# Kernel tuning notes

Measured on AMD Instinct MI355X. Metric: run time of the kernel, lower is better.

Reference implementation:

```python
import jax, jax.numpy as jnp
import numpy as np

B, C, D, K = 65536, 128, 32, 10
EPS = 1e-12


def setup_inputs() -> dict:
    key = jax.random.key(0)
    k1, k2, k3, k4 = jax.random.split(key, 4)
    data = jax.random.normal(k1, (B, D), dtype=jnp.float32)
    mu = jax.random.normal(k2, (C, D), dtype=jnp.float32)
    # S_inv must be symmetric positive definite (inverse covariance per cluster)
    A = 0.1 * jax.random.normal(k3, (C, D, D), dtype=jnp.float32)
    S_inv = jnp.einsum('cij,ckj->cik', A, A) + jnp.eye(D, dtype=jnp.float32)[None]
    # one-hot class assignment per cluster (int32), as stored in the module
    cls = jax.random.randint(k4, (C,), 0, K)
    cluster_labels = jax.nn.one_hot(cls, K, dtype=jnp.int32)
    return {"data": data, "mu": mu, "S_inv": S_inv, "cluster_labels": cluster_labels}


def reference(data, mu, S_inv, cluster_labels):
    # Mahalanobis distance d2[b,c] = (z_b - mu_c)^T S_inv_c (z_b - mu_c),
    # expanded to avoid a [B, C, D] diff tensor.
    zz = data[:, :, None] * data[:, None, :]            # [B, D, D]
    t1 = jnp.einsum('bde,cde->bc', zz, S_inv)           # z' Sinv z
    Sm = jnp.einsum('cde,ce->cd', S_inv, mu)            # [C, D]
    t2 = data @ Sm.T                                    # z' Sinv mu  [B, C]
    t3 = jnp.einsum('cd,cd->c', mu, Sm)                 # mu' Sinv mu [C]
    d2 = t1 - 2.0 * t2 + t3[None, :]                    # [B, C]
    Gamma = jnp.exp(-0.5 * d2)                          # Gaussian activation
    # defuzzify_batch: normalize activations, project through one-hot labels
    norm_gamma = Gamma / (jnp.sum(Gamma, axis=1, keepdims=True) + EPS)
    label_scores = norm_gamma @ cluster_labels.astype(jnp.float32)  # [B, K]
    preds = jnp.argmax(label_scores, axis=1)
    clusters = jnp.argmax(Gamma, axis=1)
    return label_scores, preds, clusters
```

## Files before the change

### kernel.cpp

```cpp
#include <hip/hip_runtime.h>
#include <cmath>

#define B_N 65536
#define C_N 128
#define D_N 32
#define K_N 10
#define EPS_F 1e-12f
#define SCALE_F (-0.72134752044448169f)

#define NKK 46
#define CHUNK_F16 4096
#define QF_N (NKK * CHUNK_F16)
#define YSTR 41

typedef _Float16 f16x8 __attribute__((ext_vector_type(8)));
typedef float    f32x16 __attribute__((ext_vector_type(16)));

__device__ __forceinline__ void mdkk(int kk, int& dA, int& e0) {
    if (kk >= 45) { dA = 0; e0 = 0; return; }
    int w = (kk >= 17) + (kk >= 30) + (kk >= 39) + (kk >= 44);
    int off = w == 0 ? 0 : (w == 1 ? 17 : (w == 2 ? 30 : (w == 3 ? 39 : 44)));
    int r = kk - off;
    dA = 2 * r;
    e0 = 2 * r + 8 * w;
}

__global__ __launch_bounds__(128) void k_prep(const float* __restrict__ S,
                                              const float* __restrict__ mu,
                                              const int* __restrict__ onehot,
                                              _Float16* __restrict__ QF,
                                              int* __restrict__ cls) {
    const int c = blockIdx.x;
    const int tid = threadIdx.x;
    __shared__ float sSm[D_N];
    __shared__ float st3;

    if (tid < D_N) {
        const float* Sr = S + (size_t)c * (D_N * D_N) + (size_t)tid * D_N;
        const float* mr = mu + (size_t)c * D_N;
        float a0 = 0.f, a1 = 0.f;
#pragma unroll
        for (int e = 0; e < D_N; e += 2) {
            a0 = fmaf(Sr[e + 0], mr[e + 0], a0);
            a1 = fmaf(Sr[e + 1], mr[e + 1], a1);
        }
        sSm[tid] = a0 + a1;
    }
    __syncthreads();
    if (tid == 0) {
        const float* mr = mu + (size_t)c * D_N;
        float a = 0.f;
#pragma unroll
        for (int d = 0; d < D_N; ++d) a = fmaf(mr[d], sSm[d], a);
        st3 = a;
        int cl = 0;
#pragma unroll
        for (int k = 0; k < K_N; ++k)
            if (onehot[c * K_N + k] != 0) cl = k;
        cls[c] = cl;
    }
    __syncthreads();

    if (tid < 2 * NKK) {
        const int kk   = tid >> 1;
        const int half = tid & 1;
        int dA, e0;
        mdkk(kk, dA, e0);
        const int d  = dA + half;
        const int ct = c >> 5;
        const size_t base = (size_t)kk * CHUNK_F16 + ct * 1024
                          + (size_t)(half * 32 + (c & 31)) * 8;
        const float* Sc = S + (size_t)c * (D_N * D_N);
        for (int j = 0; j < 8; ++j) {
            const int e = e0 + j;
            float q = 0.f;
            if (kk < 45 && d <= e && e <= 32) {
                float v;
                if (e < 32)      v = Sc[d * D_N + e] * (d == e ? 1.f : 2.f);
                else if (d < 32) v = -2.f * sSm[d];
                else             v = st3;
                q = SCALE_F * v;
            }
            _Float16 h = (_Float16)q;
            QF[base + j]       = h;
            QF[base + 512 + j] = (_Float16)(q - (float)h);
        }
    }
}

__device__ __forceinline__ void gl_lds16(const void* g, void* l) {
    __builtin_amdgcn_global_load_lds(
        (const __attribute__((address_space(1))) unsigned int*)g,
        (__attribute__((address_space(3))) unsigned int*)l, 16, 0, 0);
}

__device__ __forceinline__ void stage_chunk(const _Float16* __restrict__ QF,
                                            _Float16* __restrict__ dst,
                                            int chunk, int wid, int lane) {
#pragma unroll
    for (int i = 0; i < 2; ++i) {
        const int slot = i * 4 + wid;
        gl_lds16(QF + (size_t)chunk * CHUNK_F16 + slot * 512 + lane * 8,
                 dst + slot * 512);
    }
}

__device__ __forceinline__ void ldy(const float* sy, int ybase, int hioff,
                                    int kk, float& yd, float (&yw)[8]) {
    int dA, e0;
    mdkk(kk, dA, e0);
    yd = sy[ybase + dA + hioff];
#pragma unroll
    for (int j = 0; j < 8; ++j) yw[j] = sy[ybase + e0 + j];
}

__device__ __forceinline__ void step_compute(const _Float16* __restrict__ buf,
                                             int lane, float yd, const float (&yw)[8],
                                             f32x16 (&acc)[4]) {
    const f16x8* qb = (const f16x8*)buf;
    f16x8 qh[4], ql[4];
#pragma unroll
    for (int ct = 0; ct < 4; ++ct) {
        qh[ct] = qb[ct * 128 + lane];
        ql[ct] = qb[ct * 128 + 64 + lane];
    }
    f16x8 ph, pl;
#pragma unroll
    for (int j = 0; j < 8; j += 2) {
        float f0 = yd * yw[j], f1 = yd * yw[j + 1];
        auto h2 = __builtin_amdgcn_cvt_pkrtz(f0, f1);
        float r0 = f0 - (float)h2[0];
        float r1 = f1 - (float)h2[1];
        auto l2 = __builtin_amdgcn_cvt_pkrtz(r0, r1);
        ph[j] = h2[0]; ph[j + 1] = h2[1];
        pl[j] = l2[0]; pl[j + 1] = l2[1];
    }
#pragma unroll
    for (int ct = 0; ct < 4; ++ct)
        acc[ct] = __builtin_amdgcn_mfma_f32_32x32x16_f16(qh[ct], ph, acc[ct], 0, 0, 0);
#pragma unroll
    for (int ct = 0; ct < 4; ++ct)
        acc[ct] = __builtin_amdgcn_mfma_f32_32x32x16_f16(ql[ct], ph, acc[ct], 0, 0, 0);
#pragma unroll
    for (int ct = 0; ct < 4; ++ct)
        acc[ct] = __builtin_amdgcn_mfma_f32_32x32x16_f16(qh[ct], pl, acc[ct], 0, 0, 0);
}

__global__ __launch_bounds__(256, 2) void k_mainv6(const float* __restrict__ data,
                                                   const _Float16* __restrict__ QF,
                                                   const int* __restrict__ clsp,
                                                   float* __restrict__ out) {
    const int tid  = threadIdx.x;
    const int lane = tid & 63;
    const int wid  = tid >> 6;
    const int b0w  = blockIdx.x * 128 + wid * 32;
    const int col  = lane & 31;
    const bool hi  = lane >= 32;

    __shared__ float sy[256 * YSTR + 64];
    __shared__ alignas(16) _Float16 qbuf[2][CHUNK_F16];
    __shared__ int lcls[C_N];
    if (tid < C_N) lcls[tid] = clsp[tid];

    const int ybase = tid * YSTR;
    {
        const float4* p0 = (const float4*)(data + (size_t)(b0w + col) * D_N);
#pragma unroll
        for (int i = 0; i < 8; ++i) {
            float4 v = p0[i];
            sy[ybase + 4 * i + 0] = v.x;
            sy[ybase + 4 * i + 1] = v.y;
            sy[ybase + 4 * i + 2] = v.z;
            sy[ybase + 4 * i + 3] = v.w;
        }
        sy[ybase + 32] = 1.f;
#pragma unroll
        for (int i = 33; i < YSTR; ++i) sy[ybase + i] = 0.f;
        if (tid < 64) sy[256 * YSTR + tid] = 0.f;
    }

    f32x16 acc[4];
#pragma unroll
    for (int ct = 0; ct < 4; ++ct)
#pragma unroll
        for (int g = 0; g < 16; ++g) acc[ct][g] = 0.f;

    stage_chunk(QF, &qbuf[0][0], 0, wid, lane);
    stage_chunk(QF, &qbuf[1][0], 1, wid, lane);
    __syncthreads();

    const int hioff = hi ? 1 : 0;
    float ydA, ywA[8], ydB, ywB[8];
    ldy(sy, ybase, hioff, 0, ydA, ywA);

#pragma clang loop unroll(disable)
    for (int t = 0; t < NKK; t += 2) {
        ldy(sy, ybase, hioff, t + 1, ydB, ywB);
        step_compute(&qbuf[0][0], lane, ydA, ywA, acc);
        __syncthreads();
        if (t + 2 < NKK) stage_chunk(QF, &qbuf[0][0], t + 2, wid, lane);
        ldy(sy, ybase, hioff, t + 2, ydA, ywA);
        step_compute(&qbuf[1][0], lane, ydB, ywB, acc);
        __syncthreads();
        if (t + 3 < NKK) stage_chunk(QF, &qbuf[1][0], t + 3, wid, lane);
    }

    const float hoff = hi ? 4.f : 0.f;
    const int* lc = lcls + (hi ? 4 : 0);
    float sum = 0.f, gmax = -1.f, gcf = 0.f;
    float a0 = 0, a1 = 0, a2 = 0, a3 = 0, a4 = 0, a5 = 0, a6 = 0, a7 = 0, a8 = 0, a9 = 0;
#pragma unroll
    for (int ct = 0; ct < 4; ++ct) {
        float psum = 0.f;
#pragma unroll
        for (int g = 0; g < 16; ++g) {
            float v = acc[ct][g];
            float gm;
            asm("v_exp_f32 %0, %1" : "=v"(gm) : "v"(v));
            const int cbase = ct * 32 + (g & 3) + 8 * (g >> 2);
            int cl = lc[cbase];
            psum += gm;
            float cf = (float)cbase + hoff;
            if (gm > gmax) { gmax = gm; gcf = cf; }
            a0 += (cl == 0) ? gm : 0.f;
            a1 += (cl == 1) ? gm : 0.f;
            a2 += (cl == 2) ? gm : 0.f;
            a3 += (cl == 3) ? gm : 0.f;
            a4 += (cl == 4) ? gm : 0.f;
            a5 += (cl == 5) ? gm : 0.f;
            a6 += (cl == 6) ? gm : 0.f;
            a7 += (cl == 7) ? gm : 0.f;
            a8 += (cl == 8) ? gm : 0.f;
            a9 += (cl == 9) ? gm : 0.f;
        }
        sum += psum;
    }

    sum += __shfl_xor(sum, 32, 64);
    {
        float om = __shfl_xor(gmax, 32, 64);
        float oc = __shfl_xor(gcf, 32, 64);
        bool take = (om > gmax) || (om == gmax && oc < gcf);
        if (take) { gmax = om; gcf = oc; }
    }
    a0 += __shfl_xor(a0, 32, 64);
    a1 += __shfl_xor(a1, 32, 64);
    a2 += __shfl_xor(a2, 32, 64);
    a3 += __shfl_xor(a3, 32, 64);
    a4 += __shfl_xor(a4, 32, 64);
    a5 += __shfl_xor(a5, 32, 64);
    a6 += __shfl_xor(a6, 32, 64);
    a7 += __shfl_xor(a7, 32, 64);
    a8 += __shfl_xor(a8, 32, 64);
    a9 += __shfl_xor(a9, 32, 64);

    if (!hi) {
        const int b = b0w + col;
        float inv = 1.0f / (sum + EPS_F);
        float ls[K_N] = {a0 * inv, a1 * inv, a2 * inv, a3 * inv, a4 * inv,
                         a5 * inv, a6 * inv, a7 * inv, a8 * inv, a9 * inv};
        float best = -1.f;
        int bk = 0;
#pragma unroll
        for (int k = 0; k < K_N; ++k)
            if (ls[k] > best) { best = ls[k]; bk = k; }
        float2* o2 = (float2*)(out + (size_t)b * K_N);
#pragma unroll
        for (int k2 = 0; k2 < K_N / 2; ++k2)
            o2[k2] = make_float2(ls[2 * k2], ls[2 * k2 + 1]);
        out[(size_t)B_N * K_N + b] = (float)bk;
        out[(size_t)B_N * K_N + B_N + b] = gcf;
    }
}

extern "C" void kernel_launch(void* const* d_in, const int* in_sizes, int n_in,
                              void* d_out, int out_size, void* d_ws, size_t ws_size,
                              hipStream_t stream) {
    const float* data   = (const float*)d_in[0];
    const float* mu     = (const float*)d_in[1];
    const float* S      = (const float*)d_in[2];
    const int*   onehot = (const int*)d_in[3];
    float* out = (float*)d_out;

    _Float16* QF  = (_Float16*)d_ws;
    int*      cls = (int*)(QF + QF_N);

    hipLaunchKernelGGL(k_prep, dim3(C_N), dim3(128), 0, stream,
                       S, mu, onehot, QF, cls);
    hipLaunchKernelGGL(k_mainv6, dim3(B_N / 128), dim3(256), 0, stream,
                       data, QF, cls, out);
}
```

Baseline: 106.6 us.

## Deepen LDS staging to four buffers with vmcnt-based partial waits

Replaces the double-buffered chunk staging with a four-slot ring that keeps up to three chunks in flight. Each step waits only on its own loads via s_waitcnt vmcnt plus a raw barrier, not a full __syncthreads drain. It also raises wave priority around the MFMA sequence. The aim is to hide global-to-LDS load latency behind matrix work, at the cost of extra LDS (which may reduce occupancy) and fragile hand-counted vmcnt values.

```diff
diff --git a/kernel.cpp b/kernel.cpp
--- a/kernel.cpp
+++ b/kernel.cpp
@@ -105,6 +105,15 @@
     }
 }
 
+template <int VM>
+__device__ __forceinline__ void sync_chunk() {
+    if constexpr (VM == 4)      asm volatile("s_waitcnt vmcnt(4)" ::: "memory");
+    else if constexpr (VM == 2) asm volatile("s_waitcnt vmcnt(2)" ::: "memory");
+    else                        asm volatile("s_waitcnt vmcnt(0)" ::: "memory");
+    __builtin_amdgcn_s_barrier();
+    __builtin_amdgcn_sched_barrier(0);
+}
+
 __device__ __forceinline__ void ldy(const float* sy, int ybase, int hioff,
                                     int kk, float& yd, float (&yw)[8]) {
     int dA, e0;
@@ -135,6 +144,7 @@
         ph[j] = h2[0]; ph[j + 1] = h2[1];
         pl[j] = l2[0]; pl[j + 1] = l2[1];
     }
+    __builtin_amdgcn_s_setprio(1);
 #pragma unroll
     for (int ct = 0; ct < 4; ++ct)
         acc[ct] = __builtin_amdgcn_mfma_f32_32x32x16_f16(qh[ct], ph, acc[ct], 0, 0, 0);
@@ -144,9 +154,10 @@
 #pragma unroll
     for (int ct = 0; ct < 4; ++ct)
         acc[ct] = __builtin_amdgcn_mfma_f32_32x32x16_f16(qh[ct], pl, acc[ct], 0, 0, 0);
-}
-
-__global__ __launch_bounds__(256, 2) void k_mainv6(const float* __restrict__ data,
+    __builtin_amdgcn_s_setprio(0);
+}
+
+__global__ __launch_bounds__(256, 2) void k_mainv7(const float* __restrict__ data,
                                                    const _Float16* __restrict__ QF,
                                                    const int* __restrict__ clsp,
                                                    float* __restrict__ out) {
@@ -158,7 +169,7 @@
     const bool hi  = lane >= 32;
 
     __shared__ float sy[256 * YSTR + 64];
-    __shared__ alignas(16) _Float16 qbuf[2][CHUNK_F16];
+    __shared__ alignas(16) _Float16 qbuf[4][CHUNK_F16];
     __shared__ int lcls[C_N];
     if (tid < C_N) lcls[tid] = clsp[tid];
 
@@ -187,6 +198,7 @@
 
     stage_chunk(QF, &qbuf[0][0], 0, wid, lane);
     stage_chunk(QF, &qbuf[1][0], 1, wid, lane);
+    stage_chunk(QF, &qbuf[2][0], 2, wid, lane);
     __syncthreads();
 
     const int hioff = hi ? 1 : 0;
@@ -194,16 +206,21 @@
     ldy(sy, ybase, hioff, 0, ydA, ywA);
 
 #pragma clang loop unroll(disable)
-    for (int t = 0; t < NKK; t += 2) {
+    for (int t = 0; t < NKK - 2; t += 2) {
         ldy(sy, ybase, hioff, t + 1, ydB, ywB);
-        step_compute(&qbuf[0][0], lane, ydA, ywA, acc);
-        __syncthreads();
-        if (t + 2 < NKK) stage_chunk(QF, &qbuf[0][0], t + 2, wid, lane);
+        sync_chunk<4>();
+        if (t + 3 < NKK) stage_chunk(QF, &qbuf[(t + 3) & 3][0], t + 3, wid, lane);
+        step_compute(&qbuf[t & 3][0], lane, ydA, ywA, acc);
         ldy(sy, ybase, hioff, t + 2, ydA, ywA);
-        step_compute(&qbuf[1][0], lane, ydB, ywB, acc);
-        __syncthreads();
-        if (t + 3 < NKK) stage_chunk(QF, &qbuf[1][0], t + 3, wid, lane);
-    }
+        sync_chunk<4>();
+        if (t + 4 < NKK) stage_chunk(QF, &qbuf[(t + 4) & 3][0], t + 4, wid, lane);
+        step_compute(&qbuf[(t + 1) & 3][0], lane, ydB, ywB, acc);
+    }
+    ldy(sy, ybase, hioff, NKK - 1, ydB, ywB);
+    sync_chunk<2>();
+    step_compute(&qbuf[(NKK - 2) & 3][0], lane, ydA, ywA, acc);
+    sync_chunk<0>();
+    step_compute(&qbuf[(NKK - 1) & 3][0], lane, ydB, ywB, acc);
 
     const float hoff = hi ? 4.f : 0.f;
     const int* lc = lcls + (hi ? 4 : 0);
@@ -287,6 +304,6 @@
 
     hipLaunchKernelGGL(k_prep, dim3(C_N), dim3(128), 0, stream,
                        S, mu, onehot, QF, cls);
-    hipLaunchKernelGGL(k_mainv6, dim3(B_N / 128), dim3(256), 0, stream,
+    hipLaunchKernelGGL(k_mainv7, dim3(B_N / 128), dim3(256), 0, stream,
                        data, QF, cls, out);
 }
```

After: 108.1 us. About the same (+1.4%).

## Split K across wave pairs with two row-groups per wave and LDS reduction

Applied to the files above, without the earlier changes.

Each wave now handles 64 rows (two 32-row MFMA tiles) over half of the K-chunks, so each Q fragment loaded from LDS feeds twice as many MFMAs. The two K-halves are summed through a shared-memory scratch exchange before the epilogue. The loop uses a single barrier per step with an explicit vmcnt wait, and raises wave priority around the MFMA block. In exchange it doubles the accumulator registers, adds a reduction pass, and leaves half the waves idle during the epilogue.

```diff
diff --git a/kernel.cpp b/kernel.cpp
--- a/kernel.cpp
+++ b/kernel.cpp
@@ -9,9 +9,13 @@
 #define SCALE_F (-0.72134752044448169f)
 
 #define NKK 46
+#define HKK 23
 #define CHUNK_F16 4096
 #define QF_N (NKK * CHUNK_F16)
-#define YSTR 41
+#define YSTR 33
+#define SY_FLOATS (128 * YSTR + 64)
+#define SY_BYTES  (SY_FLOATS * 4)
+#define SMEM_BYTES (2 * 8448 * 4)
 
 typedef _Float16 f16x8 __attribute__((ext_vector_type(8)));
 typedef float    f32x16 __attribute__((ext_vector_type(16)));
@@ -105,8 +109,8 @@
     }
 }
 
-__device__ __forceinline__ void ldy(const float* sy, int ybase, int hioff,
-                                    int kk, float& yd, float (&yw)[8]) {
+__device__ __forceinline__ void ldy1(const float* sy, int ybase, int hioff,
+                                     int kk, float& yd, float (&yw)[8]) {
     int dA, e0;
     mdkk(kk, dA, e0);
     yd = sy[ybase + dA + hioff];
@@ -114,17 +118,8 @@
     for (int j = 0; j < 8; ++j) yw[j] = sy[ybase + e0 + j];
 }
 
-__device__ __forceinline__ void step_compute(const _Float16* __restrict__ buf,
-                                             int lane, float yd, const float (&yw)[8],
-                                             f32x16 (&acc)[4]) {
-    const f16x8* qb = (const f16x8*)buf;
-    f16x8 qh[4], ql[4];
-#pragma unroll
-    for (int ct = 0; ct < 4; ++ct) {
-        qh[ct] = qb[ct * 128 + lane];
-        ql[ct] = qb[ct * 128 + 64 + lane];
-    }
-    f16x8 ph, pl;
+__device__ __forceinline__ void mkphi(float yd, const float (&yw)[8],
+                                      f16x8& ph, f16x8& pl) {
 #pragma unroll
     for (int j = 0; j < 8; j += 2) {
         float f0 = yd * yw[j], f1 = yd * yw[j + 1];
@@ -135,141 +130,212 @@
         ph[j] = h2[0]; ph[j + 1] = h2[1];
         pl[j] = l2[0]; pl[j + 1] = l2[1];
     }
-#pragma unroll
-    for (int ct = 0; ct < 4; ++ct)
-        acc[ct] = __builtin_amdgcn_mfma_f32_32x32x16_f16(qh[ct], ph, acc[ct], 0, 0, 0);
-#pragma unroll
-    for (int ct = 0; ct < 4; ++ct)
-        acc[ct] = __builtin_amdgcn_mfma_f32_32x32x16_f16(ql[ct], ph, acc[ct], 0, 0, 0);
-#pragma unroll
-    for (int ct = 0; ct < 4; ++ct)
-        acc[ct] = __builtin_amdgcn_mfma_f32_32x32x16_f16(qh[ct], pl, acc[ct], 0, 0, 0);
-}
-
-__global__ __launch_bounds__(256, 2) void k_mainv6(const float* __restrict__ data,
+}
+
+__device__ __forceinline__ void step2(const _Float16* __restrict__ buf, int lane,
+                                      float yd0, const float (&yw0)[8],
+                                      float yd1, const float (&yw1)[8],
+                                      f32x16 (&acc0)[4], f32x16 (&acc1)[4]) {
+    const f16x8* qbv = (const f16x8*)buf;
+    f16x8 qh[4], ql[4];
+#pragma unroll
+    for (int ct = 0; ct < 4; ++ct) {
+        qh[ct] = qbv[ct * 128 + lane];
+        ql[ct] = qbv[ct * 128 + 64 + lane];
+    }
+    f16x8 ph0, pl0, ph1, pl1;
+    mkphi(yd0, yw0, ph0, pl0);
+    mkphi(yd1, yw1, ph1, pl1);
+    __builtin_amdgcn_s_setprio(1);
+#pragma unroll
+    for (int ct = 0; ct < 4; ++ct)
+        acc0[ct] = __builtin_amdgcn_mfma_f32_32x32x16_f16(qh[ct], ph0, acc0[ct], 0, 0, 0);
+#pragma unroll
+    for (int ct = 0; ct < 4; ++ct)
+        acc1[ct] = __builtin_amdgcn_mfma_f32_32x32x16_f16(qh[ct], ph1, acc1[ct], 0, 0, 0);
+#pragma unroll
+    for (int ct = 0; ct < 4; ++ct)
+        acc0[ct] = __builtin_amdgcn_mfma_f32_32x32x16_f16(ql[ct], ph0, acc0[ct], 0, 0, 0);
+#pragma unroll
+    for (int ct = 0; ct < 4; ++ct)
+        acc1[ct] = __builtin_amdgcn_mfma_f32_32x32x16_f16(ql[ct], ph1, acc1[ct], 0, 0, 0);
+#pragma unroll
+    for (int ct = 0; ct < 4; ++ct)
+        acc0[ct] = __builtin_amdgcn_mfma_f32_32x32x16_f16(qh[ct], pl0, acc0[ct], 0, 0, 0);
+#pragma unroll
+    for (int ct = 0; ct < 4; ++ct)
+        acc1[ct] = __builtin_amdgcn_mfma_f32_32x32x16_f16(qh[ct], pl1, acc1[ct], 0, 0, 0);
+    __builtin_amdgcn_s_setprio(0);
+}
+
+__global__ __launch_bounds__(256, 2) void k_mainv8(const float* __restrict__ data,
                                                    const _Float16* __restrict__ QF,
                                                    const int* __restrict__ clsp,
                                                    float* __restrict__ out) {
     const int tid  = threadIdx.x;
     const int lane = tid & 63;
     const int wid  = tid >> 6;
-    const int b0w  = blockIdx.x * 128 + wid * 32;
+    const int pair = wid >> 1;
+    const int kh   = wid & 1;
     const int col  = lane & 31;
     const bool hi  = lane >= 32;
-
-    __shared__ float sy[256 * YSTR + 64];
-    __shared__ alignas(16) _Float16 qbuf[2][CHUNK_F16];
+    const int rbase = blockIdx.x * 128 + pair * 64;
+
+    __shared__ __attribute__((aligned(16))) char smem[SMEM_BYTES];
     __shared__ int lcls[C_N];
+    float*    sy = (float*)smem;
+    _Float16* qb = (_Float16*)(smem + SY_BYTES);
+
     if (tid < C_N) lcls[tid] = clsp[tid];
-
-    const int ybase = tid * YSTR;
-    {
-        const float4* p0 = (const float4*)(data + (size_t)(b0w + col) * D_N);
+    if (tid < 128) {
+        const float4* p0 = (const float4*)(data + (size_t)(blockIdx.x * 128 + tid) * D_N);
+        const int yb = tid * YSTR;
 #pragma unroll
         for (int i = 0; i < 8; ++i) {
             float4 v = p0[i];
-            sy[ybase + 4 * i + 0] = v.x;
-            sy[ybase + 4 * i + 1] = v.y;
-            sy[ybase + 4 * i + 2] = v.z;
-            sy[ybase + 4 * i + 3] = v.w;
-        }
-        sy[ybase + 32] = 1.f;
-#pragma unroll
-        for (int i = 33; i < YSTR; ++i) sy[ybase + i] = 0.f;
-        if (tid < 64) sy[256 * YSTR + tid] = 0.f;
-    }
-
-    f32x16 acc[4];
-#pragma unroll
-    for (int ct = 0; ct < 4; ++ct)
-#pragma unroll
-        for (int g = 0; g < 16; ++g) acc[ct][g] = 0.f;
-
-    stage_chunk(QF, &qbuf[0][0], 0, wid, lane);
-    stage_chunk(QF, &qbuf[1][0], 1, wid, lane);
+            sy[yb + 4 * i + 0] = v.x;
+            sy[yb + 4 * i + 1] = v.y;
+            sy[yb + 4 * i + 2] = v.z;
+            sy[yb + 4 * i + 3] = v.w;
+        }
+        sy[yb + 32] = 1.f;
+    }
+    if (tid < 64) sy[128 * YSTR + tid] = 0.f;
+
+    f32x16 acc0[4], acc1[4];
+#pragma unroll
+    for (int ct = 0; ct < 4; ++ct)
+#pragma unroll
+        for (int g = 0; g < 16; ++g) { acc0[ct][g] = 0.f; acc1[ct][g] = 0.f; }
+
+    stage_chunk(QF, qb + 0 * CHUNK_F16, 0,   wid, lane);
+    stage_chunk(QF, qb + 2 * CHUNK_F16, HKK, wid, lane);
     __syncthreads();
 
     const int hioff = hi ? 1 : 0;
-    float ydA, ywA[8], ydB, ywB[8];
-    ldy(sy, ybase, hioff, 0, ydA, ywA);
+    const int yb0 = (pair * 64 + col) * YSTR;
+    const int yb1 = yb0 + 32 * YSTR;
 
 #pragma clang loop unroll(disable)
-    for (int t = 0; t < NKK; t += 2) {
-        ldy(sy, ybase, hioff, t + 1, ydB, ywB);
-        step_compute(&qbuf[0][0], lane, ydA, ywA, acc);
-        __syncthreads();
-        if (t + 2 < NKK) stage_chunk(QF, &qbuf[0][0], t + 2, wid, lane);
-        ldy(sy, ybase, hioff, t + 2, ydA, ywA);
-        step_compute(&qbuf[1][0], lane, ydB, ywB, acc);
-        __syncthreads();
-        if (t + 3 < NKK) stage_chunk(QF, &qbuf[1][0], t + 3, wid, lane);
+    for (int t = 0; t < HKK; ++t) {
+        asm volatile("s_waitcnt vmcnt(0)" ::: "memory");
+        __builtin_amdgcn_s_barrier();
+        __builtin_amdgcn_sched_barrier(0);
+        if (t + 1 < HKK) {
+            stage_chunk(QF, qb + (((t + 1) & 1)) * CHUNK_F16, t + 1, wid, lane);
+            stage_chunk(QF, qb + (2 + ((t + 1) & 1)) * CHUNK_F16, HKK + t + 1, wid, lane);
+        }
+        const int kk = kh * HKK + t;
+        float yd0, yw0[8], yd1, yw1[8];
+        ldy1(sy, yb0, hioff, kk, yd0, yw0);
+        ldy1(sy, yb1, hioff, kk, yd1, yw1);
+        step2(qb + (kh * 2 + (t & 1)) * CHUNK_F16, lane, yd0, yw0, yd1, yw1, acc0, acc1);
+    }
+
+    __syncthreads();
+    float* scr = (float*)smem + pair * 8448;
+    if (kh == 1) {
+#pragma unroll
+        for (int bg = 0; bg < 2; ++bg) {
+            const f32x16* ap = bg ? acc1 : acc0;
+#pragma unroll
+            for (int ct = 0; ct < 4; ++ct)
+#pragma unroll
+                for (int gq = 0; gq < 4; ++gq) {
+                    const int g4 = bg * 16 + ct * 4 + gq;
+                    const int fo = lane * 132 + (((g4 + 2 * lane) & 31) << 2);
+                    *(float4*)(scr + fo) = make_float4(ap[ct][4 * gq + 0], ap[ct][4 * gq + 1],
+                                                       ap[ct][4 * gq + 2], ap[ct][4 * gq + 3]);
+                }
+        }
+    }
+    __syncthreads();
+    if (kh != 0) return;
+
+#pragma unroll
+    for (int bg = 0; bg < 2; ++bg) {
+        f32x16* ap = bg ? acc1 : acc0;
+#pragma unroll
+        for (int ct = 0; ct < 4; ++ct)
+#pragma unroll
+            for (int gq = 0; gq < 4; ++gq) {
+                const int g4 = bg * 16 + ct * 4 + gq;
+                const int fo = lane * 132 + (((g4 + 2 * lane) & 31) << 2);
+                float4 v = *(const float4*)(scr + fo);
+                ap[ct][4 * gq + 0] += v.x; ap[ct][4 * gq + 1] += v.y;
+                ap[ct][4 * gq + 2] += v.z; ap[ct][4 * gq + 3] += v.w;
+            }
     }
 
     const float hoff = hi ? 4.f : 0.f;
     const int* lc = lcls + (hi ? 4 : 0);
-    float sum = 0.f, gmax = -1.f, gcf = 0.f;
-    float a0 = 0, a1 = 0, a2 = 0, a3 = 0, a4 = 0, a5 = 0, a6 = 0, a7 = 0, a8 = 0, a9 = 0;
-#pragma unroll
-    for (int ct = 0; ct < 4; ++ct) {
-        float psum = 0.f;
-#pragma unroll
-        for (int g = 0; g < 16; ++g) {
-            float v = acc[ct][g];
-            float gm;
-            asm("v_exp_f32 %0, %1" : "=v"(gm) : "v"(v));
-            const int cbase = ct * 32 + (g & 3) + 8 * (g >> 2);
-            int cl = lc[cbase];
-            psum += gm;
-            float cf = (float)cbase + hoff;
-            if (gm > gmax) { gmax = gm; gcf = cf; }
-            a0 += (cl == 0) ? gm : 0.f;
-            a1 += (cl == 1) ? gm : 0.f;
-            a2 += (cl == 2) ? gm : 0.f;
-            a3 += (cl == 3) ? gm : 0.f;
-            a4 += (cl == 4) ? gm : 0.f;
-            a5 += (cl == 5) ? gm : 0.f;
-            a6 += (cl == 6) ? gm : 0.f;
-            a7 += (cl == 7) ? gm : 0.f;
-            a8 += (cl == 8) ? gm : 0.f;
-            a9 += (cl == 9) ? gm : 0.f;
-        }
-        sum += psum;
-    }
-
-    sum += __shfl_xor(sum, 32, 64);
-    {
-        float om = __shfl_xor(gmax, 32, 64);
-        float oc = __shfl_xor(gcf, 32, 64);
-        bool take = (om > gmax) || (om == gmax && oc < gcf);
-        if (take) { gmax = om; gcf = oc; }
-    }
-    a0 += __shfl_xor(a0, 32, 64);
-    a1 += __shfl_xor(a1, 32, 64);
-    a2 += __shfl_xor(a2, 32, 64);
-    a3 += __shfl_xor(a3, 32, 64);
-    a4 += __shfl_xor(a4, 32, 64);
-    a5 += __shfl_xor(a5, 32, 64);
-    a6 += __shfl_xor(a6, 32, 64);
-    a7 += __shfl_xor(a7, 32, 64);
-    a8 += __shfl_xor(a8, 32, 64);
-    a9 += __shfl_xor(a9, 32, 64);
-
-    if (!hi) {
-        const int b = b0w + col;
-        float inv = 1.0f / (sum + EPS_F);
-        float ls[K_N] = {a0 * inv, a1 * inv, a2 * inv, a3 * inv, a4 * inv,
-                         a5 * inv, a6 * inv, a7 * inv, a8 * inv, a9 * inv};
-        float best = -1.f;
-        int bk = 0;
-#pragma unroll
-        for (int k = 0; k < K_N; ++k)
-            if (ls[k] > best) { best = ls[k]; bk = k; }
-        float2* o2 = (float2*)(out + (size_t)b * K_N);
-#pragma unroll
-        for (int k2 = 0; k2 < K_N / 2; ++k2)
-            o2[k2] = make_float2(ls[2 * k2], ls[2 * k2 + 1]);
-        out[(size_t)B_N * K_N + b] = (float)bk;
-        out[(size_t)B_N * K_N + B_N + b] = gcf;
+#pragma unroll
+    for (int bg = 0; bg < 2; ++bg) {
+        const f32x16* ap = bg ? acc1 : acc0;
+        float sum = 0.f, gmax = -1.f, gcf = 0.f;
+        float a0 = 0, a1 = 0, a2 = 0, a3 = 0, a4 = 0, a5 = 0, a6 = 0, a7 = 0, a8 = 0, a9 = 0;
+#pragma unroll
+        for (int ct = 0; ct < 4; ++ct) {
+            float psum = 0.f;
+#pragma unroll
+            for (int g = 0; g < 16; ++g) {
+                float v = ap[ct][g];
+                float gm;
+                asm("v_exp_f32 %0, %1" : "=v"(gm) : "v"(v));
+                const int cbase = ct * 32 + (g & 3) + 8 * (g >> 2);
+                int cl = lc[cbase];
+                psum += gm;
+                float cf = (float)cbase + hoff;
+                if (gm > gmax) { gmax = gm; gcf = cf; }
+                a0 += (cl == 0) ? gm : 0.f;
+                a1 += (cl == 1) ? gm : 0.f;
+                a2 += (cl == 2) ? gm : 0.f;
+                a3 += (cl == 3) ? gm : 0.f;
+                a4 += (cl == 4) ? gm : 0.f;
+                a5 += (cl == 5) ? gm : 0.f;
+                a6 += (cl == 6) ? gm : 0.f;
+                a7 += (cl == 7) ? gm : 0.f;
+                a8 += (cl == 8) ? gm : 0.f;
+                a9 += (cl == 9) ? gm : 0.f;
+            }
+            sum += psum;
+        }
+
+        sum += __shfl_xor(sum, 32, 64);
+        {
+            float om = __shfl_xor(gmax, 32, 64);
+            float oc = __shfl_xor(gcf, 32, 64);
+            bool take = (om > gmax) || (om == gmax && oc < gcf);
+            if (take) { gmax = om; gcf = oc; }
+        }
+        a0 += __shfl_xor(a0, 32, 64);
+        a1 += __shfl_xor(a1, 32, 64);
+        a2 += __shfl_xor(a2, 32, 64);
+        a3 += __shfl_xor(a3, 32, 64);
+        a4 += __shfl_xor(a4, 32, 64);
+        a5 += __shfl_xor(a5, 32, 64);
+        a6 += __shfl_xor(a6, 32, 64);
+        a7 += __shfl_xor(a7, 32, 64);
+        a8 += __shfl_xor(a8, 32, 64);
+        a9 += __shfl_xor(a9, 32, 64);
+
+        if (!hi) {
+            const int b = rbase + bg * 32 + col;
+            float inv = 1.0f / (sum + EPS_F);
+            float ls[K_N] = {a0 * inv, a1 * inv, a2 * inv, a3 * inv, a4 * inv,
+                             a5 * inv, a6 * inv, a7 * inv, a8 * inv, a9 * inv};
+            float best = -1.f;
+            int bk = 0;
+#pragma unroll
+            for (int k = 0; k < K_N; ++k)
+                if (ls[k] > best) { best = ls[k]; bk = k; }
+            float2* o2 = (float2*)(out + (size_t)b * K_N);
+#pragma unroll
+            for (int k2 = 0; k2 < K_N / 2; ++k2)
+                o2[k2] = make_float2(ls[2 * k2], ls[2 * k2 + 1]);
+            out[(size_t)B_N * K_N + b] = (float)bk;
+            out[(size_t)B_N * K_N + B_N + b] = gcf;
+        }
     }
 }
 
@@ -287,6 +353,6 @@
 
     hipLaunchKernelGGL(k_prep, dim3(C_N), dim3(128), 0, stream,
                        S, mu, onehot, QF, cls);
-    hipLaunchKernelGGL(k_mainv6, dim3(B_N / 128), dim3(256), 0, stream,
+    hipLaunchKernelGGL(k_mainv8, dim3(B_N / 128), dim3(256), 0, stream,
                        data, QF, cls, out);
 }
```

After: 115.2 us. +8.1%, slower.

## Use four-slot LDS ring with register double-buffered operands and one barrier per step

Applied to the files above, without the earlier changes.

Replaces the two-buffer chunk loop with a four-slot LDS ring. Each step waits on outstanding loads and hits one barrier, issues the async stage two chunks ahead, and preloads the next step's Q fragments and y values into registers before running the current MFMAs. MFMA issue priority is raised during compute. NKK is padded to 48 so the loop unrolls evenly by four, and the y stride shrinks to 33. This trades more LDS and registers, plus two extra padded chunks of MFMA work, for less barrier stall and better overlap of LDS reads with matrix math.

```diff
diff --git a/kernel.cpp b/kernel.cpp
--- a/kernel.cpp
+++ b/kernel.cpp
@@ -8,10 +8,10 @@
 #define EPS_F 1e-12f
 #define SCALE_F (-0.72134752044448169f)
 
-#define NKK 46
+#define NKK 48
 #define CHUNK_F16 4096
 #define QF_N (NKK * CHUNK_F16)
-#define YSTR 41
+#define YSTR 33
 
 typedef _Float16 f16x8 __attribute__((ext_vector_type(8)));
 typedef float    f32x16 __attribute__((ext_vector_type(16)));
@@ -114,39 +114,61 @@
     for (int j = 0; j < 8; ++j) yw[j] = sy[ybase + e0 + j];
 }
 
-__device__ __forceinline__ void step_compute(const _Float16* __restrict__ buf,
-                                             int lane, float yd, const float (&yw)[8],
-                                             f32x16 (&acc)[4]) {
-    const f16x8* qb = (const f16x8*)buf;
-    f16x8 qh[4], ql[4];
-#pragma unroll
-    for (int ct = 0; ct < 4; ++ct) {
-        qh[ct] = qb[ct * 128 + lane];
-        ql[ct] = qb[ct * 128 + 64 + lane];
-    }
-    f16x8 ph, pl;
-#pragma unroll
-    for (int j = 0; j < 8; j += 2) {
-        float f0 = yd * yw[j], f1 = yd * yw[j + 1];
+__device__ __forceinline__ void mkphi(float yd, const float (&yw)[8],
+                                      f16x8& ph, f16x8& pl) {
+    union { unsigned int w[4]; f16x8 v; } H, L;
+#pragma unroll
+    for (int p = 0; p < 4; ++p) {
+        float f0 = yd * yw[2 * p], f1 = yd * yw[2 * p + 1];
         auto h2 = __builtin_amdgcn_cvt_pkrtz(f0, f1);
         float r0 = f0 - (float)h2[0];
         float r1 = f1 - (float)h2[1];
         auto l2 = __builtin_amdgcn_cvt_pkrtz(r0, r1);
-        ph[j] = h2[0]; ph[j + 1] = h2[1];
-        pl[j] = l2[0]; pl[j + 1] = l2[1];
-    }
+        __builtin_memcpy(&H.w[p], &h2, 4);
+        __builtin_memcpy(&L.w[p], &l2, 4);
+    }
+    ph = H.v;
+    pl = L.v;
+}
+
+template <int SN, int SS, int P>
+__device__ __forceinline__ void phase_t(int t, const _Float16* __restrict__ QF,
+                                        _Float16* __restrict__ qb,
+                                        const float* __restrict__ sy,
+                                        int ybase, int hioff, int wid, int lane,
+                                        f16x8 (&qh)[2][4], f16x8 (&ql)[2][4],
+                                        float (&yd)[2], float (&yw)[2][8],
+                                        f32x16 (&acc)[4]) {
+    asm volatile("s_waitcnt vmcnt(0)" ::: "memory");
+    __builtin_amdgcn_s_barrier();
+    __builtin_amdgcn_sched_barrier(0);
+    if (t + 2 < NKK)
+        stage_chunk(QF, qb + SS * CHUNK_F16, t + 2, wid, lane);
+    if (t + 1 < NKK) {
+        const f16x8* qn = (const f16x8*)(qb + SN * CHUNK_F16);
+#pragma unroll
+        for (int ct = 0; ct < 4; ++ct) {
+            qh[P ^ 1][ct] = qn[ct * 128 + lane];
+            ql[P ^ 1][ct] = qn[ct * 128 + 64 + lane];
+        }
+        ldy(sy, ybase, hioff, t + 1, yd[P ^ 1], yw[P ^ 1]);
+    }
+    f16x8 ph, pl;
+    mkphi(yd[P], yw[P], ph, pl);
+    __builtin_amdgcn_s_setprio(1);
 #pragma unroll
     for (int ct = 0; ct < 4; ++ct)
-        acc[ct] = __builtin_amdgcn_mfma_f32_32x32x16_f16(qh[ct], ph, acc[ct], 0, 0, 0);
+        acc[ct] = __builtin_amdgcn_mfma_f32_32x32x16_f16(qh[P][ct], ph, acc[ct], 0, 0, 0);
 #pragma unroll
     for (int ct = 0; ct < 4; ++ct)
-        acc[ct] = __builtin_amdgcn_mfma_f32_32x32x16_f16(ql[ct], ph, acc[ct], 0, 0, 0);
+        acc[ct] = __builtin_amdgcn_mfma_f32_32x32x16_f16(ql[P][ct], ph, acc[ct], 0, 0, 0);
 #pragma unroll
     for (int ct = 0; ct < 4; ++ct)
-        acc[ct] = __builtin_amdgcn_mfma_f32_32x32x16_f16(qh[ct], pl, acc[ct], 0, 0, 0);
-}
-
-__global__ __launch_bounds__(256, 2) void k_mainv6(const float* __restrict__ data,
+        acc[ct] = __builtin_amdgcn_mfma_f32_32x32x16_f16(qh[P][ct], pl, acc[ct], 0, 0, 0);
+    __builtin_amdgcn_s_setprio(0);
+}
+
+__global__ __launch_bounds__(256, 2) void k_mainv9(const float* __restrict__ data,
                                                    const _Float16* __restrict__ QF,
                                                    const int* __restrict__ clsp,
                                                    float* __restrict__ out) {
@@ -158,7 +180,7 @@
     const bool hi  = lane >= 32;
 
     __shared__ float sy[256 * YSTR + 64];
-    __shared__ alignas(16) _Float16 qbuf[2][CHUNK_F16];
+    __shared__ alignas(16) _Float16 qb[4 * CHUNK_F16];
     __shared__ int lcls[C_N];
     if (tid < C_N) lcls[tid] = clsp[tid];
 
@@ -174,8 +196,6 @@
             sy[ybase + 4 * i + 3] = v.w;
         }
         sy[ybase + 32] = 1.f;
-#pragma unroll
-        for (int i = 33; i < YSTR; ++i) sy[ybase + i] = 0.f;
         if (tid < 64) sy[256 * YSTR + tid] = 0.f;
     }
 
@@ -185,24 +205,29 @@
 #pragma unroll
         for (int g = 0; g < 16; ++g) acc[ct][g] = 0.f;
 
-    stage_chunk(QF, &qbuf[0][0], 0, wid, lane);
-    stage_chunk(QF, &qbuf[1][0], 1, wid, lane);
+    stage_chunk(QF, qb + 0 * CHUNK_F16, 0, wid, lane);
+    stage_chunk(QF, qb + 1 * CHUNK_F16, 1, wid, lane);
     __syncthreads();
 
     const int hioff = hi ? 1 : 0;
-    float ydA, ywA[8], ydB, ywB[8];
-    ldy(sy, ybase, hioff, 0, ydA, ywA);
+    f16x8 qh[2][4], ql[2][4];
+    float yd[2], yw[2][8];
+    {
+        const f16x8* q0 = (const f16x8*)qb;
+#pragma unroll
+        for (int ct = 0; ct < 4; ++ct) {
+            qh[0][ct] = q0[ct * 128 + lane];
+            ql[0][ct] = q0[ct * 128 + 64 + lane];
+        }
+        ldy(sy, ybase, hioff, 0, yd[0], yw[0]);
+    }
 
 #pragma clang loop unroll(disable)
-    for (int t = 0; t < NKK; t += 2) {
-        ldy(sy, ybase, hioff, t + 1, ydB, ywB);
-        step_compute(&qbuf[0][0], lane, ydA, ywA, acc);
-        __syncthreads();
-        if (t + 2 < NKK) stage_chunk(QF, &qbuf[0][0], t + 2, wid, lane);
-        ldy(sy, ybase, hioff, t + 2, ydA, ywA);
-        step_compute(&qbuf[1][0], lane, ydB, ywB, acc);
-        __syncthreads();
-        if (t + 3 < NKK) stage_chunk(QF, &qbuf[1][0], t + 3, wid, lane);
+    for (int t = 0; t < NKK; t += 4) {
+        phase_t<1, 2, 0>(t + 0, QF, qb, sy, ybase, hioff, wid, lane, qh, ql, yd, yw, acc);
+        phase_t<2, 3, 1>(t + 1, QF, qb, sy, ybase, hioff, wid, lane, qh, ql, yd, yw, acc);
+        phase_t<3, 0, 0>(t + 2, QF, qb, sy, ybase, hioff, wid, lane, qh, ql, yd, yw, acc);
+        phase_t<0, 1, 1>(t + 3, QF, qb, sy, ybase, hioff, wid, lane, qh, ql, yd, yw, acc);
     }
 
     const float hoff = hi ? 4.f : 0.f;
@@ -287,6 +312,6 @@
 
     hipLaunchKernelGGL(k_prep, dim3(C_N), dim3(128), 0, stream,
                        S, mu, onehot, QF, cls);
-    hipLaunchKernelGGL(k_mainv6, dim3(B_N / 128), dim3(256), 0, stream,
+    hipLaunchKernelGGL(k_mainv9, dim3(B_N / 128), dim3(256), 0, stream,
                        data, QF, cls, out);
 }
```

After: 109.9 us. 3.1% more time.
